# Kernel optimization log

Hardware: AMD Instinct MI355X
Metric: run time of the kernel (lower is better)

## Reference

```python
import jax, jax.numpy as jnp
import numpy as np

N, DEG, F_IN, F_OUT = 100000, 16, 128, 128
E = N * DEG


def setup_inputs() -> dict:
    key = jax.random.key(0)
    k0, k1, k2, k3 = jax.random.split(key, 4)
    x = jax.random.normal(k0, (N, F_IN), dtype=jnp.float32)
    # ragged neighbor list flattened: each node has DEG neighbors (sorted segment ids)
    neighbor_feats = jax.random.normal(k1, (E, F_IN), dtype=jnp.float32)
    segment_ids = jnp.repeat(jnp.arange(N, dtype=jnp.int32), DEG)
    # nn.Linear(in, out, bias=False) weights, stored [out, in] as in torch
    Wx = jax.random.normal(k2, (F_OUT, F_IN), dtype=jnp.float32) / np.float32(np.sqrt(F_IN))
    Wn = jax.random.normal(k3, (F_OUT, F_IN), dtype=jnp.float32) / np.float32(np.sqrt(F_IN))
    return {"x": x, "neighbor_feats": neighbor_feats, "segment_ids": segment_ids,
            "Wx": Wx, "Wn": Wn}


def reference(x, neighbor_feats, segment_ids, Wx, Wn):
    n_nodes = x.shape[0]
    # MeanAggregator: per-node mean over its neighbor rows (segment mean)
    sums = jax.ops.segment_sum(neighbor_feats, segment_ids, num_segments=n_nodes)
    counts = jax.ops.segment_sum(
        jnp.ones((neighbor_feats.shape[0],), dtype=x.dtype), segment_ids,
        num_segments=n_nodes)
    f = sums / jnp.maximum(counts, 1.0)[:, None]  # [N, F_IN]
    # tranx(x) + trann(f)
    x_out = x @ Wx.T + f @ Wn.T                   # [N, F_OUT]
    # neighbor = [tranx(n) for n in neighbor], flattened
    nb_out = neighbor_feats @ Wx.T                # [E, F_OUT]
    return x_out, nb_out
```

## Files before the change

### kernel.cpp

```cpp
#include <hip/hip_runtime.h>
#include <stdint.h>
#include <stddef.h>

#define N_NODES 100000
#define F_DIM   128
#define DEG     16
#define N_EDGES (N_NODES*DEG)
#define ROWS_PER_TILE 128
#define N_TILES (N_EDGES/ROWS_PER_TILE)
#define NODES_PER_TILE (ROWS_PER_TILE/DEG)
#define GRID_BLOCKS 2048
#define BLOCK_THREADS 256
#define G_STRIDE 132

typedef __bf16 bf16;
typedef __bf16 bf16x8 __attribute__((ext_vector_type(8)));
typedef float  f32x4  __attribute__((ext_vector_type(4)));

__device__ __forceinline__ int swz(int row, int col) {
  return row*128 + (col ^ ((row & 7) << 3));
}

__device__ __forceinline__ bf16x8 cvt8(f32x4 a, f32x4 b) {
  bf16x8 v;
  v[0]=(bf16)a[0]; v[1]=(bf16)a[1]; v[2]=(bf16)a[2]; v[3]=(bf16)a[3];
  v[4]=(bf16)b[0]; v[5]=(bf16)b[1]; v[6]=(bf16)b[2]; v[7]=(bf16)b[3];
  return v;
}

__device__ __forceinline__ bf16x8 load_frag_g(const float* __restrict__ p) {
  f32x4 a = *(const f32x4*)p;
  f32x4 b = *(const f32x4*)(p + 4);
  return cvt8(a, b);
}

__global__ __launch_bounds__(BLOCK_THREADS, 2)
void feattrans_kernel(const float* __restrict__ x,
                      const float* __restrict__ nb,
                      const float* __restrict__ Wx,
                      const float* __restrict__ Wn,
                      float* __restrict__ out)
{
  __shared__ bf16  w_lds[2*128*128];
  __shared__ float g_lds[16*G_STRIDE];

  const int tid  = threadIdx.x;
  const int wave = tid >> 6;
  const int lane = tid & 63;
  const int l15  = lane & 15;
  const int lk   = lane >> 4;

  #pragma unroll
  for (int it = 0; it < 16; ++it) {
    int idx = it * BLOCK_THREADS + tid;
    int mat = idx >> 11;
    int rem = idx & 2047;
    int row = rem >> 4;
    int g   = rem & 15;
    const float* src = (mat ? Wn : Wx) + row*128 + g*8;
    bf16x8 v = load_frag_g(src);
    *(bf16x8*)&w_lds[mat*16384 + swz(row, g*8)] = v;
  }
  __syncthreads();

  float* out_x  = out;
  float* out_nb = out + (size_t)N_NODES * F_DIM;

  for (int tile = blockIdx.x; tile < N_TILES; tile += GRID_BLOCKS) {
    const size_t erow0 = (size_t)tile * ROWS_PER_TILE;

    bf16x8 afr[2][4];
    #pragma unroll
    for (int mt = 0; mt < 2; ++mt)
      #pragma unroll
      for (int ks = 0; ks < 4; ++ks) {
        const float* p = nb + (erow0 + wave*32 + mt*16 + l15) * F_DIM + ks*32 + lk*8;
        afr[mt][ks] = load_frag_g(p);
      }

    f32x4 acc[2][8] = {};
    #pragma unroll
    for (int nt = 0; nt < 8; ++nt) {
      #pragma unroll
      for (int ks = 0; ks < 4; ++ks) {
        bf16x8 bfr = *(bf16x8*)&w_lds[swz(nt*16 + l15, ks*32 + lk*8)];
        acc[0][nt] = __builtin_amdgcn_mfma_f32_16x16x32_bf16(afr[0][ks], bfr, acc[0][nt], 0, 0, 0);
        acc[1][nt] = __builtin_amdgcn_mfma_f32_16x16x32_bf16(afr[1][ks], bfr, acc[1][nt], 0, 0, 0);
      }
    }
    #pragma unroll
    for (int mt = 0; mt < 2; ++mt)
      #pragma unroll
      for (int nt = 0; nt < 8; ++nt)
        #pragma unroll
        for (int i = 0; i < 4; ++i) {
          size_t r = erow0 + wave*32 + mt*16 + lk*4 + i;
          out_nb[r * F_DIM + nt*16 + l15] = acc[mt][nt][i];
        }

    #pragma unroll
    for (int mt = 0; mt < 2; ++mt) {
      f32x4 a2[8] = {};
      #pragma unroll
      for (int nt = 0; nt < 8; ++nt)
        #pragma unroll
        for (int ks = 0; ks < 4; ++ks) {
          bf16x8 bfr = *(bf16x8*)&w_lds[16384 + swz(nt*16 + l15, ks*32 + lk*8)];
          a2[nt] = __builtin_amdgcn_mfma_f32_16x16x32_bf16(afr[mt][ks], bfr, a2[nt], 0, 0, 0);
        }
      const int gnode = 2*wave + mt;
      #pragma unroll
      for (int nt = 0; nt < 8; ++nt) {
        float s = a2[nt][0] + a2[nt][1] + a2[nt][2] + a2[nt][3];
        s += __shfl_xor(s, 16, 64);
        s += __shfl_xor(s, 32, 64);
        s *= (1.0f / DEG);
        if ((nt >> 1) == lk)
          g_lds[gnode*G_STRIDE + nt*16 + l15] = s;
      }
    }

    const int nodebase = tile * NODES_PER_TILE;
    int xrow = nodebase + l15;
    if (xrow > N_NODES - 1) xrow = N_NODES - 1;
    bf16x8 xfr[4];
    #pragma unroll
    for (int ks = 0; ks < 4; ++ks)
      xfr[ks] = load_frag_g(x + (size_t)xrow * F_DIM + ks*32 + lk*8);

    __syncthreads();

    f32x4 xacc[2] = {};
    #pragma unroll
    for (int j = 0; j < 2; ++j) {
      int n = (wave*2 + j)*16 + l15;
      #pragma unroll
      for (int ks = 0; ks < 4; ++ks) {
        bf16x8 bx = *(bf16x8*)&w_lds[swz(n, ks*32 + lk*8)];
        xacc[j] = __builtin_amdgcn_mfma_f32_16x16x32_bf16(xfr[ks], bx, xacc[j], 0, 0, 0);
      }
    }
    #pragma unroll
    for (int j = 0; j < 2; ++j)
      #pragma unroll
      for (int i = 0; i < 4; ++i) {
        int r = lk*4 + i;
        if (r < NODES_PER_TILE) {
          float g = g_lds[r*G_STRIDE + (wave*2 + j)*16 + l15];
          out_x[(size_t)(nodebase + r) * F_DIM + (wave*2 + j)*16 + l15] = xacc[j][i] + g;
        }
      }

    __syncthreads();
  }
}

extern "C" void kernel_launch(void* const* d_in, const int* in_sizes, int n_in,
                              void* d_out, int out_size, void* d_ws, size_t ws_size,
                              hipStream_t stream) {
  const float* x  = (const float*)d_in[0];
  const float* nb = (const float*)d_in[1];
  const float* Wx = (const float*)d_in[3];
  const float* Wn = (const float*)d_in[4];
  float* out = (float*)d_out;

  feattrans_kernel<<<dim3(GRID_BLOCKS), dim3(BLOCK_THREADS), 0, stream>>>(x, nb, Wx, Wn, out);
}
```

Baseline: 363.6 us.

## Keep neighbor-mean results in registers and drop per-tile block barriers

Each wave now computes the full x @ Wx^T tile for all 8 output column groups itself. The aggregated neighbor projection stays in registers and is added directly, instead of being staged through shared memory between two __syncthreads. The grid moves to 2500 blocks that each process a contiguous run of tiles, with the loop left unrolled once. The cost is four times the redundant x-projection MFMAs per wave (every wave repeats the same x GEMM) and only a quarter of the lanes doing stores, in exchange for removing both barriers and the LDS round trip.

Measured after the change: 380.4 us. 4.6% more time.

```diff
diff --git a/kernel.cpp b/kernel.cpp
--- a/kernel.cpp
+++ b/kernel.cpp
@@ -9,9 +9,9 @@
 #define ROWS_PER_TILE 128
 #define N_TILES (N_EDGES/ROWS_PER_TILE)
 #define NODES_PER_TILE (ROWS_PER_TILE/DEG)
-#define GRID_BLOCKS 2048
+#define GRID_BLOCKS 2500
+#define TILES_PER_BLOCK (N_TILES/GRID_BLOCKS)
 #define BLOCK_THREADS 256
-#define G_STRIDE 132
 
 typedef __bf16 bf16;
 typedef __bf16 bf16x8 __attribute__((ext_vector_type(8)));
@@ -41,8 +41,7 @@
                       const float* __restrict__ Wn,
                       float* __restrict__ out)
 {
-  __shared__ bf16  w_lds[2*128*128];
-  __shared__ float g_lds[16*G_STRIDE];
+  __shared__ bf16 w_lds[2*128*128];
 
   const int tid  = threadIdx.x;
   const int wave = tid >> 6;
@@ -66,7 +65,9 @@
   float* out_x  = out;
   float* out_nb = out + (size_t)N_NODES * F_DIM;
 
-  for (int tile = blockIdx.x; tile < N_TILES; tile += GRID_BLOCKS) {
+  #pragma unroll 1
+  for (int t = 0; t < TILES_PER_BLOCK; ++t) {
+    const int tile = blockIdx.x * TILES_PER_BLOCK + t;
     const size_t erow0 = (size_t)tile * ROWS_PER_TILE;
 
     bf16x8 afr[2][4];
@@ -98,6 +99,7 @@
           out_nb[r * F_DIM + nt*16 + l15] = acc[mt][nt][i];
         }
 
+    float g[2][8];
     #pragma unroll
     for (int mt = 0; mt < 2; ++mt) {
       f32x4 a2[8] = {};
@@ -108,15 +110,12 @@
           bf16x8 bfr = *(bf16x8*)&w_lds[16384 + swz(nt*16 + l15, ks*32 + lk*8)];
           a2[nt] = __builtin_amdgcn_mfma_f32_16x16x32_bf16(afr[mt][ks], bfr, a2[nt], 0, 0, 0);
         }
-      const int gnode = 2*wave + mt;
       #pragma unroll
       for (int nt = 0; nt < 8; ++nt) {
         float s = a2[nt][0] + a2[nt][1] + a2[nt][2] + a2[nt][3];
         s += __shfl_xor(s, 16, 64);
         s += __shfl_xor(s, 32, 64);
-        s *= (1.0f / DEG);
-        if ((nt >> 1) == lk)
-          g_lds[gnode*G_STRIDE + nt*16 + l15] = s;
+        g[mt][nt] = s * (1.0f / DEG);
       }
     }
 
@@ -128,30 +127,27 @@
     for (int ks = 0; ks < 4; ++ks)
       xfr[ks] = load_frag_g(x + (size_t)xrow * F_DIM + ks*32 + lk*8);
 
-    __syncthreads();
-
-    f32x4 xacc[2] = {};
+    f32x4 xacc[8] = {};
     #pragma unroll
-    for (int j = 0; j < 2; ++j) {
-      int n = (wave*2 + j)*16 + l15;
+    for (int nt = 0; nt < 8; ++nt) {
       #pragma unroll
       for (int ks = 0; ks < 4; ++ks) {
-        bf16x8 bx = *(bf16x8*)&w_lds[swz(n, ks*32 + lk*8)];
-        xacc[j] = __builtin_amdgcn_mfma_f32_16x16x32_bf16(xfr[ks], bx, xacc[j], 0, 0, 0);
+        bf16x8 bx = *(bf16x8*)&w_lds[swz(nt*16 + l15, ks*32 + lk*8)];
+        xacc[nt] = __builtin_amdgcn_mfma_f32_16x16x32_bf16(xfr[ks], bx, xacc[nt], 0, 0, 0);
       }
     }
-    #pragma unroll
-    for (int j = 0; j < 2; ++j)
+
+    const int r0 = 2*wave;
+    const bool hi = (wave & 1);
+    if (lk == (wave >> 1)) {
       #pragma unroll
-      for (int i = 0; i < 4; ++i) {
-        int r = lk*4 + i;
-        if (r < NODES_PER_TILE) {
-          float g = g_lds[r*G_STRIDE + (wave*2 + j)*16 + l15];
-          out_x[(size_t)(nodebase + r) * F_DIM + (wave*2 + j)*16 + l15] = xacc[j][i] + g;
-        }
+      for (int nt = 0; nt < 8; ++nt) {
+        float v0 = hi ? xacc[nt][2] : xacc[nt][0];
+        float v1 = hi ? xacc[nt][3] : xacc[nt][1];
+        out_x[(size_t)(nodebase + r0    ) * F_DIM + nt*16 + l15] = v0 + g[0][nt];
+        out_x[(size_t)(nodebase + r0 + 1) * F_DIM + nt*16 + l15] = v1 + g[1][nt];
       }
-
-    __syncthreads();
+    }
   }
 }
 
```

## Prefetch next tile's neighbor rows, vectorize stores via transposed MFMA, double-buffer LDS

Applied to the files above, without the earlier changes.

Sets the grid to 2500 blocks so each block handles exactly 5 tiles in a fully unrolled loop. The next tile's neighbor fragments are prefetched into a second register set while the current tile computes. MFMA operands are swapped so each lane holds four consecutive output columns, which lets the nb and x outputs be written as 16-byte vector stores instead of scalar ones. The g_lds buffer is double-buffered, which removes the trailing barrier. This costs more registers for the doubled A fragments, which may hurt occupancy under the 2-blocks launch bound.

After: 356.4 us. -2.0%, faster.

```diff
diff --git a/kernel.cpp b/kernel.cpp
--- a/kernel.cpp
+++ b/kernel.cpp
@@ -9,7 +9,8 @@
 #define ROWS_PER_TILE 128
 #define N_TILES (N_EDGES/ROWS_PER_TILE)
 #define NODES_PER_TILE (ROWS_PER_TILE/DEG)
-#define GRID_BLOCKS 2048
+#define GRID_BLOCKS 2500
+#define TILES_PER_BLOCK (N_TILES/GRID_BLOCKS)
 #define BLOCK_THREADS 256
 #define G_STRIDE 132
 
@@ -42,7 +43,7 @@
                       float* __restrict__ out)
 {
   __shared__ bf16  w_lds[2*128*128];
-  __shared__ float g_lds[16*G_STRIDE];
+  __shared__ float g_lds[2][NODES_PER_TILE][G_STRIDE];
 
   const int tid  = threadIdx.x;
   const int wave = tid >> 6;
@@ -66,17 +67,32 @@
   float* out_x  = out;
   float* out_nb = out + (size_t)N_NODES * F_DIM;
 
-  for (int tile = blockIdx.x; tile < N_TILES; tile += GRID_BLOCKS) {
-    const size_t erow0 = (size_t)tile * ROWS_PER_TILE;
+  const int bid = blockIdx.x;
 
-    bf16x8 afr[2][4];
+  bf16x8 afr[2][2][4];
+
+  {
+    const size_t erow0 = (size_t)bid * ROWS_PER_TILE;
     #pragma unroll
     for (int mt = 0; mt < 2; ++mt)
       #pragma unroll
-      for (int ks = 0; ks < 4; ++ks) {
-        const float* p = nb + (erow0 + wave*32 + mt*16 + l15) * F_DIM + ks*32 + lk*8;
-        afr[mt][ks] = load_frag_g(p);
-      }
+      for (int ks = 0; ks < 4; ++ks)
+        afr[0][mt][ks] = load_frag_g(nb + (erow0 + wave*32 + mt*16 + l15) * F_DIM + ks*32 + lk*8);
+  }
+
+  #pragma unroll
+  for (int t = 0; t < TILES_PER_BLOCK; ++t) {
+    const int cur = t & 1, nxt = cur ^ 1;
+    const int tile = bid + t * GRID_BLOCKS;
+    const size_t erow0 = (size_t)tile * ROWS_PER_TILE;
+    const int nodebase = tile * NODES_PER_TILE;
+
+    int xrow = nodebase + l15;
+    if (xrow > N_NODES - 1) xrow = N_NODES - 1;
+    bf16x8 xfr[4];
+    #pragma unroll
+    for (int ks = 0; ks < 4; ++ks)
+      xfr[ks] = load_frag_g(x + (size_t)xrow * F_DIM + ks*32 + lk*8);
 
     f32x4 acc[2][8] = {};
     #pragma unroll
@@ -84,19 +100,15 @@
       #pragma unroll
       for (int ks = 0; ks < 4; ++ks) {
         bf16x8 bfr = *(bf16x8*)&w_lds[swz(nt*16 + l15, ks*32 + lk*8)];
-        acc[0][nt] = __builtin_amdgcn_mfma_f32_16x16x32_bf16(afr[0][ks], bfr, acc[0][nt], 0, 0, 0);
-        acc[1][nt] = __builtin_amdgcn_mfma_f32_16x16x32_bf16(afr[1][ks], bfr, acc[1][nt], 0, 0, 0);
+        acc[0][nt] = __builtin_amdgcn_mfma_f32_16x16x32_bf16(bfr, afr[cur][0][ks], acc[0][nt], 0, 0, 0);
+        acc[1][nt] = __builtin_amdgcn_mfma_f32_16x16x32_bf16(bfr, afr[cur][1][ks], acc[1][nt], 0, 0, 0);
       }
     }
     #pragma unroll
     for (int mt = 0; mt < 2; ++mt)
       #pragma unroll
       for (int nt = 0; nt < 8; ++nt)
-        #pragma unroll
-        for (int i = 0; i < 4; ++i) {
-          size_t r = erow0 + wave*32 + mt*16 + lk*4 + i;
-          out_nb[r * F_DIM + nt*16 + l15] = acc[mt][nt][i];
-        }
+        *(f32x4*)(out_nb + (erow0 + wave*32 + mt*16 + l15) * F_DIM + nt*16 + lk*4) = acc[mt][nt];
 
     #pragma unroll
     for (int mt = 0; mt < 2; ++mt) {
@@ -106,7 +118,7 @@
         #pragma unroll
         for (int ks = 0; ks < 4; ++ks) {
           bf16x8 bfr = *(bf16x8*)&w_lds[16384 + swz(nt*16 + l15, ks*32 + lk*8)];
-          a2[nt] = __builtin_amdgcn_mfma_f32_16x16x32_bf16(afr[mt][ks], bfr, a2[nt], 0, 0, 0);
+          a2[nt] = __builtin_amdgcn_mfma_f32_16x16x32_bf16(afr[cur][mt][ks], bfr, a2[nt], 0, 0, 0);
         }
       const int gnode = 2*wave + mt;
       #pragma unroll
@@ -115,43 +127,41 @@
         s += __shfl_xor(s, 16, 64);
         s += __shfl_xor(s, 32, 64);
         s *= (1.0f / DEG);
-        if ((nt >> 1) == lk)
-          g_lds[gnode*G_STRIDE + nt*16 + l15] = s;
+        if (lk == (nt >> 1))
+          g_lds[cur][gnode][nt*16 + l15] = s;
       }
     }
 
-    const int nodebase = tile * NODES_PER_TILE;
-    int xrow = nodebase + l15;
-    if (xrow > N_NODES - 1) xrow = N_NODES - 1;
-    bf16x8 xfr[4];
-    #pragma unroll
-    for (int ks = 0; ks < 4; ++ks)
-      xfr[ks] = load_frag_g(x + (size_t)xrow * F_DIM + ks*32 + lk*8);
+    if (t < TILES_PER_BLOCK - 1) {
+      const size_t erowN = erow0 + (size_t)GRID_BLOCKS * ROWS_PER_TILE;
+      #pragma unroll
+      for (int mt = 0; mt < 2; ++mt)
+        #pragma unroll
+        for (int ks = 0; ks < 4; ++ks)
+          afr[nxt][mt][ks] = load_frag_g(nb + (erowN + wave*32 + mt*16 + l15) * F_DIM + ks*32 + lk*8);
+    }
 
     __syncthreads();
 
     f32x4 xacc[2] = {};
     #pragma unroll
     for (int j = 0; j < 2; ++j) {
-      int n = (wave*2 + j)*16 + l15;
+      const int nt = 2*wave + j;
       #pragma unroll
       for (int ks = 0; ks < 4; ++ks) {
-        bf16x8 bx = *(bf16x8*)&w_lds[swz(n, ks*32 + lk*8)];
-        xacc[j] = __builtin_amdgcn_mfma_f32_16x16x32_bf16(xfr[ks], bx, xacc[j], 0, 0, 0);
+        bf16x8 bx = *(bf16x8*)&w_lds[swz(nt*16 + l15, ks*32 + lk*8)];
+        xacc[j] = __builtin_amdgcn_mfma_f32_16x16x32_bf16(bx, xfr[ks], xacc[j], 0, 0, 0);
       }
     }
-    #pragma unroll
-    for (int j = 0; j < 2; ++j)
+    if (l15 < NODES_PER_TILE) {
       #pragma unroll
-      for (int i = 0; i < 4; ++i) {
-        int r = lk*4 + i;
-        if (r < NODES_PER_TILE) {
-          float g = g_lds[r*G_STRIDE + (wave*2 + j)*16 + l15];
-          out_x[(size_t)(nodebase + r) * F_DIM + (wave*2 + j)*16 + l15] = xacc[j][i] + g;
-        }
+      for (int j = 0; j < 2; ++j) {
+        const int nt = 2*wave + j;
+        f32x4 g4 = *(f32x4*)&g_lds[cur][l15][nt*16 + lk*4];
+        f32x4 v  = xacc[j] + g4;
+        *(f32x4*)(out_x + (size_t)(nodebase + l15) * F_DIM + nt*16 + lk*4) = v;
       }
-
-    __syncthreads();
+    }
   }
 }
 
```
